# Performance work log

Measured on AMD Instinct MI355X. Metric: run time of the kernel, lower is better.

Reference implementation:

```python
import math
import jax, jax.numpy as jnp
import numpy as np

S = 2048
HIDDEN = 5120
H = 16              # num_local_heads (128 global heads / TP=8)
NOPE, ROPE, V = 128, 64, 128
QK = NOPE + ROPE    # 192 (module pads to 256; zero-pad is a mathematical no-op)
QLORA, KVLORA = 1536, 512
EPS = 1e-6
BASE, FACTOR = 10000.0, 40.0
BETA_FAST, BETA_SLOW = 32.0, 1.0
ORIG_MAX = 4096
MSCALE = MSCALE_ALL = 0.707


def _yarn_get_mscale(scale, mscale):
    if scale <= 1:
        return 1.0
    return 0.1 * mscale * math.log(scale) + 1.0


SCALING = QK ** -0.5 * _yarn_get_mscale(FACTOR, MSCALE_ALL) ** 2
COS_SIN_MSCALE = _yarn_get_mscale(FACTOR, MSCALE) / _yarn_get_mscale(FACTOR, MSCALE_ALL)


def _yarn_inv_freq():
    half = ROPE // 2
    i = np.arange(half, dtype=np.float64)
    pos_freqs = BASE ** (2.0 * i / ROPE)
    inv_extra = 1.0 / pos_freqs
    inv_interp = 1.0 / (FACTOR * pos_freqs)

    def corr_dim(n_rot):
        return ROPE * math.log(ORIG_MAX / (n_rot * 2 * math.pi)) / (2 * math.log(BASE))

    low = max(math.floor(corr_dim(BETA_FAST)), 0)
    high = min(math.ceil(corr_dim(BETA_SLOW)), ROPE - 1)
    ramp = np.clip((i - low) / max(high - low, 1e-3), 0.0, 1.0)
    inv_freq_mask = 1.0 - ramp  # 1 -> extrapolation, 0 -> interpolation
    inv_freq = inv_interp * (1.0 - inv_freq_mask) + inv_extra * inv_freq_mask
    return jnp.asarray(inv_freq, dtype=jnp.float32)


INV_FREQ = _yarn_inv_freq()  # [ROPE/2]


def _apply_rope(x, cos, sin):
    # non-neox (interleaved pairs): x [S, heads, ROPE], cos/sin [S, ROPE/2]
    x1 = x[..., 0::2]
    x2 = x[..., 1::2]
    c = cos[:, None, :]
    s = sin[:, None, :]
    o1 = x1 * c - x2 * s
    o2 = x2 * c + x1 * s
    return jnp.stack([o1, o2], axis=-1).reshape(x.shape)


def _rms_norm(x, w):
    var = jnp.mean(x.astype(jnp.float32) ** 2, axis=-1, keepdims=True)
    return (x.astype(jnp.float32) * jax.lax.rsqrt(var + EPS)).astype(x.dtype) * w


def setup_inputs() -> dict:
    key = jax.random.key(0)
    ks = jax.random.split(key, 8)
    sd = 0.02
    return {
        'positions': jnp.arange(S, dtype=jnp.int64 if jax.config.jax_enable_x64 else jnp.int32),
        'hidden_states': jax.random.normal(ks[0], (S, HIDDEN), jnp.float32),
        'w_q_a': jax.random.normal(ks[1], (HIDDEN, QLORA), jnp.float32) * sd,
        'q_a_ln_w': jnp.ones((QLORA,), jnp.float32),
        'w_q_b': jax.random.normal(ks[2], (QLORA, H * QK), jnp.float32) * sd,
        'w_kv_a': jax.random.normal(ks[3], (HIDDEN, KVLORA + ROPE), jnp.float32) * sd,
        'kv_a_ln_w': jnp.ones((KVLORA,), jnp.float32),
        'w_kv_b': jax.random.normal(ks[4], (KVLORA, H * (NOPE + V)), jnp.float32) * sd,
        'w_o': jax.random.normal(ks[5], (H * V, HIDDEN), jnp.float32) * sd,
    }


def reference(positions, hidden_states, w_q_a, q_a_ln_w, w_q_b, w_kv_a, kv_a_ln_w, w_kv_b, w_o):
    # Q low-rank path: q_a_proj -> RMSNorm -> q_b_proj
    q = hidden_states @ w_q_a                       # [S, QLORA]
    q = _rms_norm(q, q_a_ln_w)
    q = (q @ w_q_b).reshape(S, H, QK)               # [S, H, 192]
    q_nope, q_pe = q[..., :NOPE], q[..., NOPE:]

    # KV latent path: shared MQA latent + decoupled rope key
    latent = hidden_states @ w_kv_a                 # [S, KVLORA+ROPE]
    kv_a = _rms_norm(latent[:, :KVLORA], kv_a_ln_w)
    k_pe = latent[:, None, KVLORA:]                 # [S, 1, ROPE]
    kv = (kv_a @ w_kv_b).reshape(S, H, NOPE + V)
    k_nope, v = kv[..., :NOPE], kv[..., NOPE:]

    # partial (decoupled) yarn RoPE on the 64-dim rope slice
    freqs = positions.astype(jnp.float32)[:, None] * INV_FREQ[None, :]
    cos = jnp.cos(freqs) * COS_SIN_MSCALE
    sin = jnp.sin(freqs) * COS_SIN_MSCALE
    q_pe = _apply_rope(q_pe, cos, sin)
    k_pe = _apply_rope(k_pe, cos, sin)

    qf = jnp.concatenate([q_nope, q_pe], axis=-1)   # [S, H, 192]
    kf = jnp.concatenate([k_nope, jnp.broadcast_to(k_pe, (S, H, ROPE))], axis=-1)

    # causal paged-attention prefill; zero-padding head dims to 256 is a no-op
    scores = jnp.einsum('qhd,khd->hqk', qf, kf) * SCALING  # [H, S, S]
    causal = jnp.tril(jnp.ones((S, S), dtype=bool))
    scores = jnp.where(causal[None], scores, -jnp.inf)
    probs = jax.nn.softmax(scores, axis=-1)
    attn = jnp.einsum('hqk,khd->qhd', probs, v).reshape(S, H * V)
    return attn @ w_o                               # [S, HIDDEN]
```

## Files before the change

kernel.cpp:

```cpp
#include <hip/hip_runtime.h>
#include <math.h>

typedef unsigned short u16;
typedef unsigned int u32;
typedef __attribute__((ext_vector_type(4))) float f32x4;
typedef __attribute__((ext_vector_type(8))) unsigned short u16x8;
typedef __attribute__((ext_vector_type(4))) unsigned short u16x4;
typedef __attribute__((ext_vector_type(4))) unsigned int u32x4;
typedef __attribute__((ext_vector_type(8))) __bf16 bf16x8;

#define DEV __device__ __forceinline__

constexpr int S = 2048;
constexpr int HIDDEN = 5120;
constexpr int H = 16;
constexpr int NOPE = 128, ROPE_D = 64, VD = 128;
constexpr int QKD = NOPE + ROPE_D;
constexpr int QLORA = 1536, KVLORA = 512;
constexpr int KVA_N = KVLORA + ROPE_D;
constexpr float SCALING = 0.11472134f;

DEV u16 f2b(float f) {
  u32 u = __builtin_bit_cast(u32, f);
  u32 r = u + 0x7FFFu + ((u >> 16) & 1u);
  return (u16)(r >> 16);
}
DEV float b2f(u16 h) { return __builtin_bit_cast(float, (u32)h << 16); }

DEV void store_out(float* p, float v) { *p = v; }
DEV void store_out(u16* p, float v) { *p = f2b(v); }

DEV void gload_lds16(const u16* g, u16* l) {
  auto* gp = (const __attribute__((address_space(1))) u16*)g;
  auto* lp = (__attribute__((address_space(3))) u16*)l;
  __builtin_amdgcn_global_load_lds(gp, lp, 16, 0, 0);
}

#define SWZ(row, col) ((col) ^ (((row) & 7) << 3))

DEV void transpose_tile(const float* __restrict__ in, u16* __restrict__ out,
                        int R, int C, int c0, int r0, int tid, float (*tl)[33]) {
  int tx = tid & 31, ty = tid >> 5;
  for (int r = ty; r < 32; r += 8)
    tl[r][tx] = in[(size_t)(r0 + r) * C + c0 + tx];
  __syncthreads();
  for (int r = ty; r < 32; r += 8)
    out[(size_t)(c0 + r) * R + r0 + tx] = f2b(tl[tx][r]);
}

__global__ __launch_bounds__(256) void k_prep(const float* __restrict__ hidden, u16* __restrict__ hs_bf,
                                              const float* __restrict__ w_q_a, u16* __restrict__ bt_qa,
                                              const float* __restrict__ w_kv_a, u16* __restrict__ bt_kva,
                                              const float* __restrict__ w_q_b, u16* __restrict__ bt_qb,
                                              const float* __restrict__ w_kv_b, u16* __restrict__ bt_kvb,
                                              float* __restrict__ cs, float* __restrict__ sn) {
  __shared__ float tl[32][33];
  int b = blockIdx.x, tid = threadIdx.x;
  if (b < 10240) {
    int i = (b * 256 + tid) * 4;
    f32x4 v = *reinterpret_cast<const f32x4*>(hidden + i);
    u16x4 o;
    o[0] = f2b(v[0]); o[1] = f2b(v[1]); o[2] = f2b(v[2]); o[3] = f2b(v[3]);
    *reinterpret_cast<u16x4*>(hs_bf + i) = o;
    return;
  }
  b -= 10240;
  if (b < 7680) {
    transpose_tile(w_q_a, bt_qa, HIDDEN, QLORA, (b % 48) * 32, (b / 48) * 32, tid, tl);
    return;
  }
  b -= 7680;
  if (b < 2880) {
    transpose_tile(w_kv_a, bt_kva, HIDDEN, KVA_N, (b % 18) * 32, (b / 18) * 32, tid, tl);
    return;
  }
  b -= 2880;
  if (b < 4608) {
    transpose_tile(w_q_b, bt_qb, QLORA, H * QKD, (b % 96) * 32, (b / 96) * 32, tid, tl);
    return;
  }
  b -= 4608;
  if (b < 2048) {
    transpose_tile(w_kv_b, bt_kvb, KVLORA, H * 256, (b % 128) * 32, (b / 128) * 32, tid, tl);
    return;
  }
  b -= 2048;
  int idx = b * 256 + tid;
  int s = idx >> 5, j = idx & 31;
  double pf = pow(10000.0, (double)j / 32.0);
  double inv_extra = 1.0 / pf;
  double inv_interp = 1.0 / (40.0 * pf);
  double twopi = 6.283185307179586476925286766559;
  double lnb2 = 2.0 * log(10000.0);
  double lowd = floor(64.0 * log(4096.0 / (32.0 * twopi)) / lnb2);
  if (lowd < 0.0) lowd = 0.0;
  double highd = ceil(64.0 * log(4096.0 / twopi) / lnb2);
  if (highd > 63.0) highd = 63.0;
  double denom = highd - lowd;
  if (denom < 0.001) denom = 0.001;
  double ramp = ((double)j - lowd) / denom;
  ramp = ramp < 0.0 ? 0.0 : (ramp > 1.0 ? 1.0 : ramp);
  float invf = (float)(inv_interp * ramp + inv_extra * (1.0 - ramp));
  float fr = (float)s * invf;
  cs[idx] = cosf(fr);
  sn[idx] = sinf(fr);
}

DEV void gemm_core(u16* Al, u16* Bl, const u16* __restrict__ A,
                   const u16* __restrict__ BT,
                   int Kstride, int Klen, int mbase, int nbase, f32x4 (*acc)[4]) {
  const int tid = threadIdx.x;
  const int lane = tid & 63, wave = tid >> 6;
  const int wr = wave >> 1, wc = wave & 1;
  const int lr = lane & 15, lk = lane >> 4;
  const int srow = wave * 32 + (lane >> 2);
  const int skoff = (((lane & 3) ^ ((lane >> 3) & 3))) * 8;
  const int swlk8 = (lk ^ ((lr >> 1) & 3)) * 8;
  const u16* aptr = A + (size_t)(mbase + srow) * Kstride + skoff;
  const u16* bptr = BT + (size_t)(nbase + srow) * Kstride + skoff;
  u16* alw = Al + wave * (32 * 32);
  u16* blw = Bl + wave * (32 * 32);

  auto STAGE = [&](int b, int kk) {
    gload_lds16(aptr + kk, alw + b * 4096);
    gload_lds16(aptr + (size_t)16 * Kstride + kk, alw + b * 4096 + 16 * 32);
    gload_lds16(bptr + kk, blw + b * 4096);
    gload_lds16(bptr + (size_t)16 * Kstride + kk, blw + b * 4096 + 16 * 32);
  };

#pragma unroll
  for (int mf = 0; mf < 4; ++mf)
#pragma unroll
    for (int nf = 0; nf < 4; ++nf) acc[mf][nf] = {0.f, 0.f, 0.f, 0.f};

  const int nt = Klen >> 5;
  STAGE(0, 0);
  STAGE(1, 32);
  for (int t = 0; t < nt; ++t) {
    const int cur = t & 1;
    if (t + 1 < nt)
      asm volatile("s_waitcnt vmcnt(4)" ::: "memory");
    else
      asm volatile("s_waitcnt vmcnt(0)" ::: "memory");
    __builtin_amdgcn_s_barrier();
    const u16* Ac = Al + cur * 4096;
    const u16* Bc = Bl + cur * 4096;
    bf16x8 af[4], bfr[4];
#pragma unroll
    for (int mf = 0; mf < 4; ++mf)
      af[mf] = *reinterpret_cast<const bf16x8*>(Ac + (wr * 64 + mf * 16 + lr) * 32 + swlk8);
#pragma unroll
    for (int nf = 0; nf < 4; ++nf)
      bfr[nf] = *reinterpret_cast<const bf16x8*>(Bc + (wc * 64 + nf * 16 + lr) * 32 + swlk8);
#pragma unroll
    for (int mf = 0; mf < 4; ++mf)
#pragma unroll
      for (int nf = 0; nf < 4; ++nf)
        acc[mf][nf] = __builtin_amdgcn_mfma_f32_16x16x32_bf16(af[mf], bfr[nf], acc[mf][nf], 0, 0, 0);
    __builtin_amdgcn_s_barrier();
    if (t + 2 < nt) STAGE(cur, (t + 2) * 32);
  }
}

template <typename OutT>
DEV void gemm_epilogue(f32x4 (*acc)[4], OutT* __restrict__ C, int N, int mbase, int nbase) {
  const int lane = threadIdx.x & 63, wave = threadIdx.x >> 6;
  const int wr = wave >> 1, wc = wave & 1;
  const int lr = lane & 15, lk = lane >> 4;
#pragma unroll
  for (int mf = 0; mf < 4; ++mf)
#pragma unroll
    for (int nf = 0; nf < 4; ++nf) {
      int col = nbase + wc * 64 + nf * 16 + lr;
      if (col < N) {
#pragma unroll
        for (int r = 0; r < 4; ++r) {
          int row = mbase + wr * 64 + mf * 16 + lk * 4 + r;
          store_out(&C[(size_t)row * N + col], acc[mf][nf][r]);
        }
      }
    }
}

__global__ __launch_bounds__(256) void k_gemm_out(const u16* __restrict__ A,
                                                  const u16* __restrict__ BT,
                                                  float* __restrict__ C) {
  __shared__ u16 Al[2 * 128 * 32];
  __shared__ u16 Bl[2 * 128 * 32];
  int id = blockIdx.x;
  int row = id & 15, col = id >> 4;
  f32x4 acc[4][4];
  gemm_core(Al, Bl, A, BT, H * VD, H * VD, row * 128, col * 128, acc);
  gemm_epilogue(acc, C, HIDDEN, row * 128, col * 128);
}

__global__ __launch_bounds__(256) void k_gemm_up(const u16* __restrict__ Aq, const u16* __restrict__ Bq,
                                                 const u16* __restrict__ Akv, const u16* __restrict__ Bkv,
                                                 const float* __restrict__ cs, const float* __restrict__ sn,
                                                 u16* __restrict__ qf, u16* __restrict__ kf,
                                                 u16* __restrict__ vt) {
  __shared__ u16 Al[2 * 128 * 32];
  __shared__ u16 Bl[2 * 128 * 32];
  int id = blockIdx.x;
  int rowb = id & 15, col = id >> 4;
  const int mbase = rowb * 128;
  const int lane = threadIdx.x & 63, wave = threadIdx.x >> 6;
  const int wr = wave >> 1, wc = wave & 1;
  const int lr = lane & 15, lk = lane >> 4;
  f32x4 acc[4][4];
  if (col < 24) {
    const int nbase = col * 128;
    gemm_core(Al, Bl, Aq, Bq, QLORA, QLORA, mbase, nbase, acc);
#pragma unroll
    for (int nf = 0; nf < 4; ++nf) {
      int colb = nbase + wc * 64 + nf * 16;
      int h = colb / 192;
      int db = colb - h * 192;
      size_t qoff = (size_t)h * S * QKD;
      if (db < NOPE) {
#pragma unroll
        for (int mf = 0; mf < 4; ++mf)
#pragma unroll
          for (int r = 0; r < 4; ++r) {
            int row = mbase + wr * 64 + mf * 16 + lk * 4 + r;
            qf[qoff + (size_t)row * QKD + db + lr] = f2b(acc[mf][nf][r]);
          }
      } else {
        int jj = (db - NOPE + lr) >> 1;
        bool odd = lr & 1;
#pragma unroll
        for (int mf = 0; mf < 4; ++mf)
#pragma unroll
          for (int r = 0; r < 4; ++r) {
            int row = mbase + wr * 64 + mf * 16 + lk * 4 + r;
            float val = acc[mf][nf][r];
            float part = __shfl_xor(val, 1);
            float c = cs[row * 32 + jj], s = sn[row * 32 + jj];
            float o = odd ? (val * c + part * s) : (val * c - part * s);
            qf[qoff + (size_t)row * QKD + db + lr] = f2b(o);
          }
      }
    }
  } else {
    const int nbase = (col - 24) * 128;
    gemm_core(Al, Bl, Akv, Bkv, KVLORA, KVLORA, mbase, nbase, acc);
#pragma unroll
    for (int nf = 0; nf < 4; ++nf) {
      int colb = nbase + wc * 64 + nf * 16;
      int h = colb >> 8;
      int db = colb & 255;
      if (db < NOPE) {
        size_t koff = (size_t)h * S * QKD;
#pragma unroll
        for (int mf = 0; mf < 4; ++mf)
#pragma unroll
          for (int r = 0; r < 4; ++r) {
            int row = mbase + wr * 64 + mf * 16 + lk * 4 + r;
            kf[koff + (size_t)row * QKD + db + lr] = f2b(acc[mf][nf][r]);
          }
      } else {
        int vtrow = h * VD + db - NOPE + lr;
#pragma unroll
        for (int mf = 0; mf < 4; ++mf) {
          int row0 = mbase + wr * 64 + mf * 16 + lk * 4;
          u16x4 pk;
          pk[0] = f2b(acc[mf][nf][0]); pk[1] = f2b(acc[mf][nf][1]);
          pk[2] = f2b(acc[mf][nf][2]); pk[3] = f2b(acc[mf][nf][3]);
          *reinterpret_cast<u16x4*>(&vt[(size_t)vtrow * S + row0]) = pk;
        }
      }
    }
  }
}

__global__ __launch_bounds__(256) void k_gemm_dp(const u16* __restrict__ A,
                                                 const u16* __restrict__ Bq,
                                                 const u16* __restrict__ Bkv,
                                                 float* __restrict__ q0, float* __restrict__ q1,
                                                 float* __restrict__ l0, float* __restrict__ l1) {
  __shared__ u16 Al[2 * 128 * 32];
  __shared__ u16 Bl[2 * 128 * 32];
  constexpr int KH = HIDDEN / 2;
  int id = blockIdx.x;
  int split = id >= 272;
  int u = id - split * 272;
  int row = u & 15, colt = u >> 4;
  const u16* As = A + split * KH;
  f32x4 acc[4][4];
  if (colt < 12) {
    gemm_core(Al, Bl, As, Bq + split * KH, HIDDEN, KH, row * 128, colt * 128, acc);
    gemm_epilogue(acc, split ? q1 : q0, QLORA, row * 128, colt * 128);
  } else {
    gemm_core(Al, Bl, As, Bkv + split * KH, HIDDEN, KH, row * 128, (colt - 12) * 128, acc);
    gemm_epilogue(acc, split ? l1 : l0, KVA_N, row * 128, (colt - 12) * 128);
  }
}

DEV void rmsnorm2_row(const float* __restrict__ x0, const float* __restrict__ x1,
                      const float* __restrict__ w, u16* __restrict__ y,
                      int ncols, int instride, int row, int tid, float* red) {
  const float* xr0 = x0 + (size_t)row * instride;
  const float* xr1 = x1 + (size_t)row * instride;
  float ss = 0.f;
  for (int i = tid * 4; i < ncols; i += 1024) {
    f32x4 a = *reinterpret_cast<const f32x4*>(xr0 + i);
    f32x4 b = *reinterpret_cast<const f32x4*>(xr1 + i);
    f32x4 v = a + b;
    ss += v[0] * v[0] + v[1] * v[1] + v[2] * v[2] + v[3] * v[3];
  }
  for (int off = 32; off > 0; off >>= 1) ss += __shfl_down(ss, off);
  if ((tid & 63) == 0) red[tid >> 6] = ss;
  __syncthreads();
  ss = red[0] + red[1] + red[2] + red[3];
  float sc = rsqrtf(ss / (float)ncols + 1e-6f);
  u16* yr = y + (size_t)row * ncols;
  for (int i = tid * 4; i < ncols; i += 1024) {
    f32x4 a = *reinterpret_cast<const f32x4*>(xr0 + i);
    f32x4 b = *reinterpret_cast<const f32x4*>(xr1 + i);
    f32x4 v = a + b;
    u16x4 o;
    o[0] = f2b(v[0] * sc * w[i]);
    o[1] = f2b(v[1] * sc * w[i + 1]);
    o[2] = f2b(v[2] * sc * w[i + 2]);
    o[3] = f2b(v[3] * sc * w[i + 3]);
    *reinterpret_cast<u16x4*>(yr + i) = o;
  }
}

__global__ __launch_bounds__(256) void k_mid(const float* __restrict__ q0, const float* __restrict__ q1,
                                             const float* __restrict__ qw, u16* __restrict__ q_ln,
                                             const float* __restrict__ l0, const float* __restrict__ l1,
                                             const float* __restrict__ kw, u16* __restrict__ kv_ln,
                                             const float* __restrict__ w_o, u16* __restrict__ bt_o,
                                             const float* __restrict__ cs, const float* __restrict__ sn,
                                             u16* __restrict__ kf) {
  __shared__ float red[4];
  __shared__ float tl[32][33];
  int b = blockIdx.x, tid = threadIdx.x;
  if (b < 2048) {
    rmsnorm2_row(q0, q1, qw, q_ln, QLORA, QLORA, b, tid, red);
    return;
  }
  if (b < 4096) {
    rmsnorm2_row(l0, l1, kw, kv_ln, KVLORA, KVA_N, b - 2048, tid, red);
    return;
  }
  if (b < 14336) {
    int u = b - 4096;
    transpose_tile(w_o, bt_o, H * VD, HIDDEN, (u % 160) * 32, (u / 160) * 32, tid, tl);
    return;
  }
  int s = b - 14336;
  for (int idx = tid; idx < H * 32; idx += 256) {
    int h = idx >> 5, j = idx & 31;
    float c = cs[s * 32 + j], si = sn[s * 32 + j];
    float k1 = l0[(size_t)s * KVA_N + KVLORA + 2 * j] + l1[(size_t)s * KVA_N + KVLORA + 2 * j];
    float k2 = l0[(size_t)s * KVA_N + KVLORA + 2 * j + 1] + l1[(size_t)s * KVA_N + KVLORA + 2 * j + 1];
    kf[((size_t)h * S + s) * QKD + NOPE + 2 * j] = f2b(k1 * c - k2 * si);
    kf[((size_t)h * S + s) * QKD + NOPE + 2 * j + 1] = f2b(k2 * c + k1 * si);
  }
}

__global__ __launch_bounds__(256) void k_attn(const u16* __restrict__ qf,
                                              const u16* __restrict__ kf,
                                              const u16* __restrict__ vt,
                                              u16* __restrict__ attn) {
  const int bidx = blockIdx.x;
  const int j = bidx & 31;
  const int h = bidx >> 5;
  const int qt = (h < 8) ? j : 31 - j;
  const int qbase = qt * 64;
  const int tid = threadIdx.x, wave = tid >> 6, lane = tid & 63;
  const int lr = lane & 15, lk = lane >> 4;
  __shared__ u16 Kl[64][192];
  __shared__ u16 Vl[128][64];

  int krow_[6], kofs_[6], vrow_[4], vofs_[4];
#pragma unroll
  for (int i = 0; i < 6; ++i) { int c = tid + i * 256; krow_[i] = c / 24; kofs_[i] = (c % 24) * 8; }
#pragma unroll
  for (int i = 0; i < 4; ++i) { int c = tid + i * 256; vrow_[i] = c >> 3; vofs_[i] = (c & 7) * 8; }
  const u16* kfh = kf + (size_t)h * S * QKD;
  const u16* vth = vt + (size_t)h * VD * S;

  bf16x8 qfrag[6];
  const u16* qrow = qf + ((size_t)h * S + qbase + wave * 16 + lr) * QKD;
#pragma unroll
  for (int d = 0; d < 6; ++d)
    qfrag[d] = *reinterpret_cast<const bf16x8*>(qrow + d * 32 + lk * 8);

  u16x8 kreg[6], vreg[4];
#pragma unroll
  for (int i = 0; i < 6; ++i)
    kreg[i] = *reinterpret_cast<const u16x8*>(kfh + (size_t)krow_[i] * QKD + kofs_[i]);
#pragma unroll
  for (int i = 0; i < 4; ++i)
    vreg[i] = *reinterpret_cast<const u16x8*>(vth + (size_t)vrow_[i] * S + vofs_[i]);

  f32x4 o[8];
#pragma unroll
  for (int f = 0; f < 8; ++f) o[f] = {0.f, 0.f, 0.f, 0.f};
  float m_ = -__builtin_inff();
  float l_ = 0.f;
  const int qrow_g = qbase + wave * 16 + lr;

  const int ktiles = qt + 1;
  for (int kt = 0; kt < ktiles; ++kt) {
    const int kbase = kt * 64;
    __builtin_amdgcn_s_barrier();
#pragma unroll
    for (int i = 0; i < 6; ++i)
      *reinterpret_cast<u16x8*>(&Kl[krow_[i]][SWZ(krow_[i], kofs_[i])]) = kreg[i];
#pragma unroll
    for (int i = 0; i < 4; ++i)
      *reinterpret_cast<u16x8*>(&Vl[vrow_[i]][SWZ(vrow_[i], vofs_[i])]) = vreg[i];
    if (kt + 1 < ktiles) {
      const int nb = kbase + 64;
#pragma unroll
      for (int i = 0; i < 6; ++i)
        kreg[i] = *reinterpret_cast<const u16x8*>(kfh + (size_t)(nb + krow_[i]) * QKD + kofs_[i]);
#pragma unroll
      for (int i = 0; i < 4; ++i)
        vreg[i] = *reinterpret_cast<const u16x8*>(vth + (size_t)vrow_[i] * S + nb + vofs_[i]);
    }
    asm volatile("s_waitcnt lgkmcnt(0)" ::: "memory");
    __builtin_amdgcn_s_barrier();

    f32x4 sacc[4];
#pragma unroll
    for (int nf = 0; nf < 4; ++nf) sacc[nf] = {0.f, 0.f, 0.f, 0.f};
    __builtin_amdgcn_s_setprio(1);
#pragma unroll
    for (int nf = 0; nf < 4; ++nf)
#pragma unroll
      for (int dk = 0; dk < 6; ++dk) {
        int krow = nf * 16 + lr;
        bf16x8 a = *reinterpret_cast<const bf16x8*>(&Kl[krow][SWZ(krow, dk * 32 + lk * 8)]);
        sacc[nf] = __builtin_amdgcn_mfma_f32_16x16x32_bf16(a, qfrag[dk], sacc[nf], 0, 0, 0);
      }
    __builtin_amdgcn_s_setprio(0);

    float p[4][4];
    float rowmax = -__builtin_inff();
#pragma unroll
    for (int nf = 0; nf < 4; ++nf)
#pragma unroll
      for (int r = 0; r < 4; ++r) {
        float v = sacc[nf][r] * SCALING;
        int kcol = kbase + nf * 16 + lk * 4 + r;
        if (kcol > qrow_g) v = -__builtin_inff();
        p[nf][r] = v;
        rowmax = fmaxf(rowmax, v);
      }
    rowmax = fmaxf(rowmax, __shfl_xor(rowmax, 16));
    rowmax = fmaxf(rowmax, __shfl_xor(rowmax, 32));

    if (!__all(rowmax - m_ <= 8.0f)) {
      float mn = fmaxf(m_, rowmax);
      float alpha = __expf(m_ - mn);
      m_ = mn;
      l_ *= alpha;
#pragma unroll
      for (int f = 0; f < 8; ++f)
#pragma unroll
        for (int r = 0; r < 4; ++r) o[f][r] *= alpha;
    }
    float rowsum = 0.f;
#pragma unroll
    for (int nf = 0; nf < 4; ++nf)
#pragma unroll
      for (int r = 0; r < 4; ++r) {
        float e = __expf(p[nf][r] - m_);
        p[nf][r] = e;
        rowsum += e;
      }
    rowsum += __shfl_xor(rowsum, 16);
    rowsum += __shfl_xor(rowsum, 32);
    l_ += rowsum;

    u32 P2[4][2];
#pragma unroll
    for (int nf = 0; nf < 4; ++nf) {
#pragma unroll
      for (int w = 0; w < 2; ++w)
        P2[nf][w] = (u32)f2b(p[nf][2 * w]) | ((u32)f2b(p[nf][2 * w + 1]) << 16);
    }

    const int srcA = lr + 32 * (lk & 1);
    const int srcB = srcA + 16;
    const bool lo = (lk < 2);
    __builtin_amdgcn_s_setprio(1);
#pragma unroll
    for (int kk = 0; kk < 2; ++kk) {
      u32 a0 = __shfl((int)P2[2 * kk][0], srcA), a1 = __shfl((int)P2[2 * kk][1], srcA);
      u32 a2 = __shfl((int)P2[2 * kk][0], srcB), a3 = __shfl((int)P2[2 * kk][1], srcB);
      u32 b0 = __shfl((int)P2[2 * kk + 1][0], srcA), b1 = __shfl((int)P2[2 * kk + 1][1], srcA);
      u32 b2 = __shfl((int)P2[2 * kk + 1][0], srcB), b3 = __shfl((int)P2[2 * kk + 1][1], srcB);
      u32x4 wsel;
      wsel[0] = lo ? a0 : b0; wsel[1] = lo ? a1 : b1;
      wsel[2] = lo ? a2 : b2; wsel[3] = lo ? a3 : b3;
      bf16x8 pvB = __builtin_bit_cast(bf16x8, wsel);
#pragma unroll
      for (int f = 0; f < 8; ++f) {
        int vrow = f * 16 + lr;
        bf16x8 a = *reinterpret_cast<const bf16x8*>(&Vl[vrow][SWZ(vrow, kk * 32 + lk * 8)]);
        o[f] = __builtin_amdgcn_mfma_f32_16x16x32_bf16(a, pvB, o[f], 0, 0, 0);
      }
    }
    __builtin_amdgcn_s_setprio(0);
  }

  float inv_l = 1.0f / l_;
#pragma unroll
  for (int f = 0; f < 8; ++f) {
    u16x4 pk;
#pragma unroll
    for (int r = 0; r < 4; ++r) pk[r] = f2b(o[f][r] * inv_l);
    *reinterpret_cast<u16x4*>(&attn[(size_t)qrow_g * (H * VD) + h * VD + f * 16 + 4 * lk]) = pk;
  }
}

extern "C" void kernel_launch(void* const* d_in, const int* in_sizes, int n_in,
                              void* d_out, int out_size, void* d_ws, size_t ws_size,
                              hipStream_t stream) {
  (void)in_sizes; (void)n_in; (void)out_size; (void)ws_size;
  const float* hidden    = (const float*)d_in[1];
  const float* w_q_a     = (const float*)d_in[2];
  const float* q_a_ln_w  = (const float*)d_in[3];
  const float* w_q_b     = (const float*)d_in[4];
  const float* w_kv_a    = (const float*)d_in[5];
  const float* kv_a_ln_w = (const float*)d_in[6];
  const float* w_kv_b    = (const float*)d_in[7];
  const float* w_o       = (const float*)d_in[8];
  float* out = (float*)d_out;

  char* ws = (char*)d_ws;
  size_t off = 0;
  auto alloc = [&](size_t bytes) {
    size_t o = off;
    off += (bytes + 255) & ~(size_t)255;
    return o;
  };
  constexpr int KVA_PAD = 640;
  size_t o_hs    = alloc((size_t)S * HIDDEN * 2);
  size_t o_btqa  = alloc((size_t)QLORA * HIDDEN * 2);
  size_t o_btkva = alloc((size_t)KVA_PAD * HIDDEN * 2);
  size_t o_btqb  = alloc((size_t)(H * QKD) * QLORA * 2);
  size_t o_btkvb = alloc((size_t)(H * 256) * KVLORA * 2);
  size_t o_qlat0 = alloc((size_t)S * QLORA * 4);
  size_t o_qlat1 = alloc((size_t)S * QLORA * 4);
  size_t o_lat0  = alloc((size_t)S * KVA_N * 4);
  size_t o_lat1  = alloc((size_t)S * KVA_N * 4);
  size_t o_qln   = alloc((size_t)S * QLORA * 2);
  size_t o_kvln  = alloc((size_t)S * KVLORA * 2);
  size_t o_kf    = alloc((size_t)H * S * QKD * 2);
  size_t o_vt    = alloc((size_t)H * VD * S * 2);
  size_t o_cs    = alloc((size_t)S * 32 * 4);
  size_t o_sn    = alloc((size_t)S * 32 * 4);

  u16* hs_bf  = (u16*)(ws + o_hs);
  u16* bt_qa  = (u16*)(ws + o_btqa);
  u16* bt_kva = (u16*)(ws + o_btkva);
  u16* bt_qb  = (u16*)(ws + o_btqb);
  u16* bt_kvb = (u16*)(ws + o_btkvb);
  float* q_lat0 = (float*)(ws + o_qlat0);
  float* q_lat1 = (float*)(ws + o_qlat1);
  float* lat0   = (float*)(ws + o_lat0);
  float* lat1   = (float*)(ws + o_lat1);
  u16* q_ln  = (u16*)(ws + o_qln);
  u16* kv_ln = (u16*)(ws + o_kvln);
  u16* kf    = (u16*)(ws + o_kf);
  u16* vt    = (u16*)(ws + o_vt);
  float* cs = (float*)(ws + o_cs);
  float* sn = (float*)(ws + o_sn);
  u16* qf   = (u16*)(ws + o_hs);
  u16* bt_o = (u16*)(ws + o_btqa);
  u16* attn = (u16*)(ws + o_qlat0);

  k_prep<<<dim3(27712), dim3(256), 0, stream>>>(hidden, hs_bf, w_q_a, bt_qa,
                                                w_kv_a, bt_kva, w_q_b, bt_qb,
                                                w_kv_b, bt_kvb, cs, sn);

  k_gemm_dp<<<dim3(544), dim3(256), 0, stream>>>(hs_bf, bt_qa, bt_kva,
                                                 q_lat0, q_lat1, lat0, lat1);

  k_mid<<<dim3(16384), dim3(256), 0, stream>>>(q_lat0, q_lat1, q_a_ln_w, q_ln,
                                               lat0, lat1, kv_a_ln_w, kv_ln,
                                               w_o, bt_o, cs, sn, kf);

  k_gemm_up<<<dim3(896), dim3(256), 0, stream>>>(q_ln, bt_qb, kv_ln, bt_kvb,
                                                 cs, sn, qf, kf, vt);

  k_attn<<<dim3(512), dim3(256), 0, stream>>>(qf, kf, vt, attn);

  k_gemm_out<<<dim3(640), dim3(256), 0, stream>>>(attn, bt_o, out);
}
```

Measured before the change: 313.3 us.

## Rewrite output projection GEMM with 256x256 tiles and 4-stage LDS pipeline

The output projection GEMM moves from 128x128 tiles on 256 threads to 256x256 tiles on 512 threads. It now uses a 4-buffer LDS ring with three tiles prefetched and explicit vmcnt waits, which raises data reuse per block and overlaps loads with MFMA work. The grid drops from 640 to 160 blocks, below what the GPU's compute units can fill, so fewer CUs are busy. The larger LDS footprint also limits occupancy.

```diff
diff --git a/kernel.cpp b/kernel.cpp
--- a/kernel.cpp
+++ b/kernel.cpp
@@ -182,16 +182,91 @@
     }
 }
 
-__global__ __launch_bounds__(256) void k_gemm_out(const u16* __restrict__ A,
+__global__ __launch_bounds__(512) void k_gemm_out(const u16* __restrict__ A,
                                                   const u16* __restrict__ BT,
                                                   float* __restrict__ C) {
-  __shared__ u16 Al[2 * 128 * 32];
-  __shared__ u16 Bl[2 * 128 * 32];
-  int id = blockIdx.x;
-  int row = id & 15, col = id >> 4;
-  f32x4 acc[4][4];
-  gemm_core(Al, Bl, A, BT, H * VD, H * VD, row * 128, col * 128, acc);
-  gemm_epilogue(acc, C, HIDDEN, row * 128, col * 128);
+  __shared__ u16 Al[4 * 256 * 32];
+  __shared__ u16 Bl[4 * 256 * 32];
+  constexpr int K = H * VD;
+  constexpr int NT = K / 32;
+  const int id = blockIdx.x;
+  const int mbase = (id & 7) * 256;
+  const int nbase = (id >> 3) * 256;
+  const int tid = threadIdx.x, lane = tid & 63, wave = tid >> 6;
+  const int wm = wave >> 2, wn = wave & 3;
+  const int lr = lane & 15, lk = lane >> 4;
+  const int srow = wave * 16 + (lane >> 2);
+  const int sgran = (lane & 3) ^ ((lane >> 2) & 3);
+  const u16* aptr = A + (size_t)(mbase + srow) * K + sgran * 8;
+  const u16* bptr = BT + (size_t)(nbase + srow) * K + sgran * 8;
+
+  auto STAGE_A = [&](int buf, int i, int t) {
+    gload_lds16(aptr + (size_t)i * 128 * K + t * 32,
+                Al + buf * 8192 + (i * 128 + wave * 16) * 32);
+  };
+  auto STAGE_B = [&](int buf, int i, int t) {
+    gload_lds16(bptr + (size_t)i * 128 * K + t * 32,
+                Bl + buf * 8192 + (i * 128 + wave * 16) * 32);
+  };
+
+  f32x4 acc[8][4];
+#pragma unroll
+  for (int mf = 0; mf < 8; ++mf)
+#pragma unroll
+    for (int nf = 0; nf < 4; ++nf) acc[mf][nf] = {0.f, 0.f, 0.f, 0.f};
+
+#pragma unroll
+  for (int t = 0; t < 3; ++t) {
+    STAGE_A(t, 0, t); STAGE_A(t, 1, t);
+    STAGE_B(t, 0, t); STAGE_B(t, 1, t);
+  }
+
+  const int rg = (lk ^ (lr & 3)) << 3;
+  for (int t = 0; t < NT; ++t) {
+    const int buf = t & 3;
+    const int rem = NT - 1 - t;
+    if (rem >= 2)      asm volatile("s_waitcnt vmcnt(8)" ::: "memory");
+    else if (rem == 1) asm volatile("s_waitcnt vmcnt(4)" ::: "memory");
+    else               asm volatile("s_waitcnt vmcnt(0)" ::: "memory");
+    __builtin_amdgcn_s_barrier();
+    const u16* Ab = Al + buf * 8192 + (wm * 128) * 32;
+    const u16* Bb = Bl + buf * 8192 + (wn * 64) * 32;
+    const int pt = t + 3;
+#pragma unroll
+    for (int mh = 0; mh < 2; ++mh) {
+      if (pt < NT) {
+        if (mh == 0) { STAGE_A(pt & 3, 0, pt); STAGE_A(pt & 3, 1, pt); }
+        else         { STAGE_B(pt & 3, 0, pt); STAGE_B(pt & 3, 1, pt); }
+      }
+      bf16x8 af[4], bf[4];
+#pragma unroll
+      for (int i = 0; i < 4; ++i)
+        af[i] = *reinterpret_cast<const bf16x8*>(Ab + ((mh * 4 + i) * 16 + lr) * 32 + rg);
+#pragma unroll
+      for (int j = 0; j < 4; ++j)
+        bf[j] = *reinterpret_cast<const bf16x8*>(Bb + (j * 16 + lr) * 32 + rg);
+      __builtin_amdgcn_s_setprio(1);
+#pragma unroll
+      for (int i = 0; i < 4; ++i)
+#pragma unroll
+        for (int j = 0; j < 4; ++j)
+          acc[mh * 4 + i][j] =
+              __builtin_amdgcn_mfma_f32_16x16x32_bf16(af[i], bf[j], acc[mh * 4 + i][j], 0, 0, 0);
+      __builtin_amdgcn_s_setprio(0);
+    }
+  }
+
+#pragma unroll
+  for (int mf = 0; mf < 8; ++mf)
+#pragma unroll
+    for (int nf = 0; nf < 4; ++nf) {
+      int col = nbase + wn * 64 + nf * 16 + lr;
+#pragma unroll
+      for (int r = 0; r < 4; ++r) {
+        int row = mbase + wm * 128 + mf * 16 + lk * 4 + r;
+        C[(size_t)row * HIDDEN + col] = acc[mf][nf][r];
+      }
+    }
 }
 
 __global__ __launch_bounds__(256) void k_gemm_up(const u16* __restrict__ Aq, const u16* __restrict__ Bq,
@@ -593,5 +668,5 @@
 
   k_attn<<<dim3(512), dim3(256), 0, stream>>>(qf, kf, vt, attn);
 
-  k_gemm_out<<<dim3(640), dim3(256), 0, stream>>>(attn, bt_o, out);
-}
+  k_gemm_out<<<dim3(160), dim3(512), 0, stream>>>(attn, bt_o, out);
+}
```

Result: slower. 335.6 us (+7.1%).

## Double-buffer K/V tiles in LDS with direct global-to-LDS async loads

Applied to the files above, without the earlier changes.

Replaces the register-staged K/V prefetch in the attention kernel with direct global-to-LDS loads (gload_lds16) into two LDS buffers, prefetching two tiles ahead and using vmcnt waits. The swizzle moves to the global source addresses so the LDS writes stay linear. This removes the VGPR round trip and the LDS store step, and aims to overlap memory with MFMA work. In exchange it doubles LDS use (about 80KB), which may reduce occupancy, and adds an extra barrier per iteration.

```diff
diff --git a/kernel.cpp b/kernel.cpp
--- a/kernel.cpp
+++ b/kernel.cpp
@@ -372,30 +372,42 @@
   const int qbase = qt * 64;
   const int tid = threadIdx.x, wave = tid >> 6, lane = tid & 63;
   const int lr = lane & 15, lk = lane >> 4;
-  __shared__ u16 Kl[64][192];
-  __shared__ u16 Vl[128][64];
-
-  int krow_[6], kofs_[6], vrow_[4], vofs_[4];
-#pragma unroll
-  for (int i = 0; i < 6; ++i) { int c = tid + i * 256; krow_[i] = c / 24; kofs_[i] = (c % 24) * 8; }
-#pragma unroll
-  for (int i = 0; i < 4; ++i) { int c = tid + i * 256; vrow_[i] = c >> 3; vofs_[i] = (c & 7) * 8; }
+  __shared__ u16 Kl2[2 * 64 * 192];
+  __shared__ u16 Vl2[2 * 128 * 64];
+
+  int krow_[6]; size_t ksrc_[6];
+#pragma unroll
+  for (int i = 0; i < 6; ++i) {
+    int off = wave * 3072 + i * 512 + lane * 8;
+    int row = off / 192, g = (off % 192) >> 3;
+    krow_[i] = row;
+    ksrc_[i] = (size_t)row * QKD + ((g ^ (row & 7)) << 3);
+  }
+  int vrow_[4]; size_t vsrc_[4];
+#pragma unroll
+  for (int i = 0; i < 4; ++i) {
+    int off = wave * 2048 + i * 512 + lane * 8;
+    int row = off / 64, g = (off % 64) >> 3;
+    vrow_[i] = row;
+    vsrc_[i] = (size_t)row * S + ((g ^ (row & 7)) << 3);
+  }
   const u16* kfh = kf + (size_t)h * S * QKD;
   const u16* vth = vt + (size_t)h * VD * S;
 
+  auto STAGE = [&](int buf, int kb) {
+#pragma unroll
+    for (int i = 0; i < 6; ++i)
+      gload_lds16(kfh + (size_t)kb * QKD + ksrc_[i], Kl2 + buf * 12288 + wave * 3072 + i * 512);
+#pragma unroll
+    for (int i = 0; i < 4; ++i)
+      gload_lds16(vth + kb + vsrc_[i], Vl2 + buf * 8192 + wave * 2048 + i * 512);
+  };
+
   bf16x8 qfrag[6];
   const u16* qrow = qf + ((size_t)h * S + qbase + wave * 16 + lr) * QKD;
 #pragma unroll
   for (int d = 0; d < 6; ++d)
     qfrag[d] = *reinterpret_cast<const bf16x8*>(qrow + d * 32 + lk * 8);
-
-  u16x8 kreg[6], vreg[4];
-#pragma unroll
-  for (int i = 0; i < 6; ++i)
-    kreg[i] = *reinterpret_cast<const u16x8*>(kfh + (size_t)krow_[i] * QKD + kofs_[i]);
-#pragma unroll
-  for (int i = 0; i < 4; ++i)
-    vreg[i] = *reinterpret_cast<const u16x8*>(vth + (size_t)vrow_[i] * S + vofs_[i]);
 
   f32x4 o[8];
 #pragma unroll
@@ -405,26 +417,18 @@
   const int qrow_g = qbase + wave * 16 + lr;
 
   const int ktiles = qt + 1;
+  STAGE(0, 0);
+  if (1 < ktiles) STAGE(1, 64);
   for (int kt = 0; kt < ktiles; ++kt) {
     const int kbase = kt * 64;
+    const int buf = kt & 1;
+    if (kt + 1 < ktiles)
+      asm volatile("s_waitcnt vmcnt(10)" ::: "memory");
+    else
+      asm volatile("s_waitcnt vmcnt(0)" ::: "memory");
     __builtin_amdgcn_s_barrier();
-#pragma unroll
-    for (int i = 0; i < 6; ++i)
-      *reinterpret_cast<u16x8*>(&Kl[krow_[i]][SWZ(krow_[i], kofs_[i])]) = kreg[i];
-#pragma unroll
-    for (int i = 0; i < 4; ++i)
-      *reinterpret_cast<u16x8*>(&Vl[vrow_[i]][SWZ(vrow_[i], vofs_[i])]) = vreg[i];
-    if (kt + 1 < ktiles) {
-      const int nb = kbase + 64;
-#pragma unroll
-      for (int i = 0; i < 6; ++i)
-        kreg[i] = *reinterpret_cast<const u16x8*>(kfh + (size_t)(nb + krow_[i]) * QKD + kofs_[i]);
-#pragma unroll
-      for (int i = 0; i < 4; ++i)
-        vreg[i] = *reinterpret_cast<const u16x8*>(vth + (size_t)vrow_[i] * S + nb + vofs_[i]);
-    }
-    asm volatile("s_waitcnt lgkmcnt(0)" ::: "memory");
-    __builtin_amdgcn_s_barrier();
+    const u16* Kb = Kl2 + buf * 12288;
+    const u16* Vb = Vl2 + buf * 8192;
 
     f32x4 sacc[4];
 #pragma unroll
@@ -435,7 +439,7 @@
 #pragma unroll
       for (int dk = 0; dk < 6; ++dk) {
         int krow = nf * 16 + lr;
-        bf16x8 a = *reinterpret_cast<const bf16x8*>(&Kl[krow][SWZ(krow, dk * 32 + lk * 8)]);
+        bf16x8 a = *reinterpret_cast<const bf16x8*>(&Kb[krow * 192 + SWZ(krow, dk * 32 + lk * 8)]);
         sacc[nf] = __builtin_amdgcn_mfma_f32_16x16x32_bf16(a, qfrag[dk], sacc[nf], 0, 0, 0);
       }
     __builtin_amdgcn_s_setprio(0);
@@ -503,11 +507,13 @@
 #pragma unroll
       for (int f = 0; f < 8; ++f) {
         int vrow = f * 16 + lr;
-        bf16x8 a = *reinterpret_cast<const bf16x8*>(&Vl[vrow][SWZ(vrow, kk * 32 + lk * 8)]);
+        bf16x8 a = *reinterpret_cast<const bf16x8*>(&Vb[vrow * 64 + SWZ(vrow, kk * 32 + lk * 8)]);
         o[f] = __builtin_amdgcn_mfma_f32_16x16x32_bf16(a, pvB, o[f], 0, 0, 0);
       }
     }
     __builtin_amdgcn_s_setprio(0);
+    __builtin_amdgcn_s_barrier();
+    if (kt + 2 < ktiles) STAGE(buf, (kt + 2) * 64);
   }
 
   float inv_l = 1.0f / l_;
```

After: 316.0 us. About the same (+0.9%).
